# Kernel tuning notes

Measured on AMD Instinct MI355X. Metric: run time of the kernel, lower is better.

Reference implementation:

```python
import jax, jax.numpy as jnp
import numpy as np
from jax import lax

# Dimensions
B, CIN, COUT = 8, 3, 3
NF = 128          # num_features
K = 9             # DISCO kernel_shape (number of filter basis functions)
HLAT, WLON = 181, 360   # in_shape == out_shape (1-degree equiangular sphere grid)
KH, KW = 5, 5     # compact lat/lon support of each DISCO basis function


def setup_inputs() -> dict:
    key = jax.random.key(0)
    ks = jax.random.split(key, 10)
    s = lambda fan: 1.0 / np.sqrt(fan)
    return {
        "x": jax.random.normal(ks[0], (B, CIN, HLAT, WLON), jnp.float32),
        # DISCO conv: latitude-dependent basis filters, quadrature weights, channel mix
        "psi": jax.random.normal(ks[1], (K, HLAT, KH, KW), jnp.float32) * s(KH * KW),
        "quad": jnp.abs(jax.random.normal(ks[2], (HLAT,), jnp.float32)) * (1.0 / HLAT)
                + jnp.sin(jnp.pi * (jnp.arange(HLAT) + 0.5) / HLAT) * (1.0 / HLAT),
        "w1": jax.random.normal(ks[3], (NF, CIN, K), jnp.float32) * s(CIN * K),
        "b1": jnp.zeros((NF,), jnp.float32),
        # standard conv2d stages
        "w2": jax.random.normal(ks[4], (NF // 2, NF, 5, 5), jnp.float32) * s(NF * 25),
        "b2": jnp.zeros((NF // 2,), jnp.float32),
        "w3": jax.random.normal(ks[5], (COUT, NF // 2, 5, 5), jnp.float32) * s(NF // 2 * 25),
        "b3": jnp.zeros((COUT,), jnp.float32),
    }


def _disco_conv_s2(x, psi, quad, w, b):
    """Discrete-continuous spherical conv: latitude-dependent gather + weighted sum.
    x: [B,C,H,W]; psi: [K,H,KH,KW]; quad: [H]; w: [O,C,K]; b: [O] -> [B,O,H,W]"""
    H, W = x.shape[-2], x.shape[-1]
    rh, rw = KH // 2, KW // 2
    xw = x * quad[None, None, :, None]                       # quadrature-weighted input
    # neighborhood indices: clipped in latitude, circular in longitude
    hi = jnp.clip(jnp.arange(H)[:, None] + jnp.arange(KH)[None, :] - rh, 0, H - 1)  # [H,KH]
    wi = (jnp.arange(W)[:, None] + jnp.arange(KW)[None, :] - rw) % W                # [W,KW]
    g = xw[:, :, hi, :]                                      # [B,C,H,KH,W]
    patches = g[:, :, :, :, wi]                              # [B,C,H,KH,W,KW]
    # project onto latitude-dependent filter basis, then mix channels per basis
    z = jnp.einsum('khij,bchiwj->bckhw', psi, patches)       # [B,C,K,H,W]
    return jnp.einsum('ock,bckhw->bohw', w, z) + b[None, :, None, None]


def _conv2d(x, w, b, pad):
    y = lax.conv_general_dilated(x, w, (1, 1), [(pad, pad), (pad, pad)],
                                 dimension_numbers=('NCHW', 'OIHW', 'NCHW'))
    return y + b[None, :, None, None]


def reference(x, psi, quad, w1, b1, w2, b2, w3, b3):
    h = jax.nn.relu(_disco_conv_s2(x, psi, quad, w1, b1))
    h = jax.nn.relu(_conv2d(h, w2, b2, 2))
    return _conv2d(h, w3, b3, 2)
```

## Files before the change

### kernel.cpp

```cpp
#include <hip/hip_runtime.h>
#include <hip/hip_bf16.h>

#define HLAT 181
#define WLON 360
#define HW (HLAT * WLON)
#define HPAD 188
#define WPAD 368
#define PCH ((size_t)HPAD * WPAD * 16)
#define W2P 372
#define PLANE2 ((size_t)HPAD * W2P * 64)
#define ZROW ((size_t)384 * 64)

typedef __attribute__((ext_vector_type(4)))  short short4v;
typedef __attribute__((ext_vector_type(8)))  short short8v;
typedef __attribute__((ext_vector_type(4)))  float f32x4;
typedef __attribute__((ext_vector_type(16))) float f32x16;

static __device__ __forceinline__ ushort bf16_hi_bits(float f) {
  union { float f; unsigned u; } c; c.f = f;
  unsigned u = c.u;
  unsigned rounded = u + 0x7FFF + ((u >> 16) & 1);
  return (ushort)(rounded >> 16);
}
static __device__ __forceinline__ float bf16_to_f(ushort b) {
  union { unsigned u; float f; } c; c.u = ((unsigned)b) << 16;
  return c.f;
}

__global__ __launch_bounds__(256) void k_tw(const float* __restrict__ w2,
                                            const float* __restrict__ w3,
                                            const float* __restrict__ w1,
                                            const float* __restrict__ b1,
                                            ushort* __restrict__ w2f,
                                            ushort* __restrict__ w1f,
                                            ushort* __restrict__ w3f) {
  int idx = blockIdx.x * 256 + threadIdx.x;
  if (idx < 51200) {
    int l   = idx & 63;
    int p   = (idx >> 6) & 1;
    int m   = (idx >> 7) & 1;
    int ch  = (idx >> 8) & 7;
    int tap = idx >> 11;
    int oc  = m * 32 + (l & 31);
    int ci0 = ch * 16 + (l >> 5) * 8;
#pragma unroll
    for (int j = 0; j < 8; ++j) {
      float f = w2[(oc * 128 + ci0 + j) * 25 + tap];
      ushort hi = bf16_hi_bits(f);
      w2f[(size_t)idx * 8 + j] = (p == 0) ? hi : bf16_hi_bits(f - bf16_to_f(hi));
    }
  }
  if (idx < 1024) {
    int l = idx & 63;
    int e = idx >> 6;
    int p  = e & 1;
    int kc = (e >> 1) & 1;
    int m  = e >> 2;
    int oc = m * 32 + (l & 31);
    int k0 = kc * 16 + (l >> 5) * 8;
#pragma unroll
    for (int j = 0; j < 8; ++j) {
      int k = k0 + j;
      float f = (k < 27) ? w1[oc * 27 + k] : (k == 27 ? b1[oc] : 0.f);
      ushort hi = bf16_hi_bits(f);
      w1f[(size_t)idx * 8 + j] = (p == 0) ? hi : bf16_hi_bits(f - bf16_to_f(hi));
    }
  }
  if (idx < 6400) {
    int l   = idx & 63;
    int p   = (idx >> 6) & 1;
    int kc  = (idx >> 7) & 1;
    int tap = idx >> 8;
    int oc  = l & 15;
    int ci0 = kc * 32 + (l >> 4) * 8;
#pragma unroll
    for (int j = 0; j < 8; ++j) {
      float f = (oc < 3) ? w3[(oc * 64 + ci0 + j) * 25 + tap] : 0.f;
      ushort hi = bf16_hi_bits(f);
      w3f[(size_t)idx * 8 + j] = (p == 0) ? hi : bf16_hi_bits(f - bf16_to_f(hi));
    }
  }
}

__global__ __launch_bounds__(256) void k_zring(ushort* __restrict__ h1s) {
  const int i = blockIdx.x * 256 + threadIdx.x;
  if (i >= 4024) return;
  int row, col;
  if (i < 736)       { row = i / 368;              col = i % 368; }
  else if (i < 2576) { int p = i - 736;  row = 183 + p / 368; col = p % 368; }
  else if (i < 2938) { int p = i - 2576; row = 2 + p % 181;   col = p / 181; }
  else               { int p = i - 2938; row = 2 + p % 181;   col = 362 + p / 181; }
  short8v z = {0, 0, 0, 0, 0, 0, 0, 0};
  short8v* d = (short8v*)(h1s + (size_t)blockIdx.y * PCH + ((size_t)row * 368 + col) * 16);
  d[0] = z; d[1] = z;
}

__global__ __launch_bounds__(256) void k_zring2(ushort* __restrict__ h2p) {
  const int i = blockIdx.x * 256 + threadIdx.x;
  if (i >= 4776) return;
  int row, col;
  if (i < 744)       { row = i / W2P;             col = i % W2P; }
  else if (i < 2604) { int p = i - 744;  row = 183 + p / W2P; col = p % W2P; }
  else               { int p = i - 2604; row = 2 + p % 181;
                       int cI = p / 181; col = (cI < 2) ? cI : 360 + cI; }
  short8v z = {0, 0, 0, 0, 0, 0, 0, 0};
  short8v* d = (short8v*)(h2p + (size_t)blockIdx.y * PLANE2 + ((size_t)row * W2P + col) * 64);
#pragma unroll
  for (int k = 0; k < 8; ++k) d[k] = z;
}

__global__ __launch_bounds__(384, 2) void k_z(const float* __restrict__ x,
    const float* __restrict__ psi, const float* __restrict__ quad,
    ushort* __restrict__ zbuf, int b0) {
  const int h = blockIdx.x;
  const int bi = blockIdx.y;
  const int b = b0 + bi;
  const int tid = threadIdx.x;
  ushort* dst = zbuf + (size_t)(bi * HLAT + h) * ZROW + (size_t)tid * 64;
  if (tid >= 360) {
    short8v zz = {0, 0, 0, 0, 0, 0, 0, 0};
    short8v* d8 = (short8v*)dst;
#pragma unroll
    for (int k = 0; k < 8; ++k) d8[k] = zz;
    return;
  }
  float z[28];
#pragma unroll
  for (int q = 0; q < 28; ++q) z[q] = 0.f;
#pragma unroll 1
  for (int i = 0; i < 5; ++i) {
    int hi = h + i - 2;
    hi = hi < 0 ? 0 : (hi >= HLAT ? HLAT - 1 : hi);
    const float qv = quad[hi];
    float pv[45];
#pragma unroll
    for (int kk = 0; kk < 9; ++kk)
#pragma unroll
      for (int j = 0; j < 5; ++j)
        pv[kk * 5 + j] = psi[((size_t)(kk * HLAT + h)) * 25 + i * 5 + j];
#pragma unroll
    for (int c = 0; c < 3; ++c) {
      const float* row = x + ((size_t)(b * 3 + c) * HLAT + hi) * WLON;
      float v[5];
#pragma unroll
      for (int j = 0; j < 5; ++j) {
        int wj = tid + j - 2;
        wj = wj < 0 ? wj + WLON : (wj >= WLON ? wj - WLON : wj);
        v[j] = row[wj] * qv;
      }
#pragma unroll
      for (int kk = 0; kk < 9; ++kk) {
        float a = 0.f;
#pragma unroll
        for (int j = 0; j < 5; ++j) a += pv[kk * 5 + j] * v[j];
        z[c * 9 + kk] += a;
      }
    }
  }
  z[27] = 1.0f;
  ushort hiv[32], lov[32];
#pragma unroll
  for (int q = 0; q < 28; ++q) {
    const ushort hb = bf16_hi_bits(z[q]);
    hiv[q] = hb;
    lov[q] = bf16_hi_bits(z[q] - bf16_to_f(hb));
  }
#pragma unroll
  for (int q = 28; q < 32; ++q) { hiv[q] = 0; lov[q] = 0; }
#pragma unroll
  for (int part = 0; part < 2; ++part)
#pragma unroll
    for (int kc = 0; kc < 2; ++kc)
#pragma unroll
      for (int half = 0; half < 2; ++half) {
        union { ushort u[8]; short8v v8; } t8;
#pragma unroll
        for (int j = 0; j < 8; ++j)
          t8.u[j] = (part == 0 ? hiv : lov)[kc * 16 + half * 8 + j];
        *(short8v*)&dst[part * 32 + kc * 16 + half * 8] = t8.v8;
      }
}

__global__ __launch_bounds__(256, 2) void k_mv(const ushort* __restrict__ zbuf,
    const ushort* __restrict__ w1f, ushort* __restrict__ h1s) {
  const int h = blockIdx.x;
  const int bi = blockIdx.y;
  const int tid = threadIdx.x;
  const int wv = tid >> 6;
  const int l = tid & 63;
  const int l31 = l & 31;
  const int q = l >> 5;
  const short8v* wf1 = (const short8v*)w1f;
  short8v A[4][2][2];
#pragma unroll
  for (int m = 0; m < 4; ++m)
#pragma unroll
    for (int kc = 0; kc < 2; ++kc)
#pragma unroll
      for (int p = 0; p < 2; ++p)
        A[m][kc][p] = wf1[(size_t)(((m * 2 + kc) * 2 + p) * 64 + l)];

  ushort* base = h1s + (size_t)bi * 16 * PCH;
  const ushort* zrow = zbuf + (size_t)(bi * HLAT + h) * ZROW;
#pragma unroll
  for (int nn = 0; nn < 3; ++nn) {
    const int n = wv * 3 + nn;
    const int px = n * 32 + l31;
    const ushort* zp = zrow + (size_t)px * 64 + q * 8;
    const short8v bh0 = *(const short8v*)(zp + 0);
    const short8v bh1 = *(const short8v*)(zp + 16);
    const short8v bl0 = *(const short8v*)(zp + 32);
    const short8v bl1 = *(const short8v*)(zp + 48);
    const bool ok = px < 360;
    const size_t pixoff = ((size_t)(h + 2) * WPAD + (px + 2)) * 16;
#pragma unroll
    for (int m = 0; m < 4; ++m) {
      f32x16 acc;
#pragma unroll
      for (int e = 0; e < 16; ++e) acc[e] = 0.f;
      acc = __builtin_amdgcn_mfma_f32_32x32x16_bf16(A[m][0][0], bh0, acc, 0, 0, 0);
      acc = __builtin_amdgcn_mfma_f32_32x32x16_bf16(A[m][0][1], bh0, acc, 0, 0, 0);
      acc = __builtin_amdgcn_mfma_f32_32x32x16_bf16(A[m][0][0], bl0, acc, 0, 0, 0);
      acc = __builtin_amdgcn_mfma_f32_32x32x16_bf16(A[m][1][0], bh1, acc, 0, 0, 0);
      acc = __builtin_amdgcn_mfma_f32_32x32x16_bf16(A[m][1][1], bh1, acc, 0, 0, 0);
      acc = __builtin_amdgcn_mfma_f32_32x32x16_bf16(A[m][1][0], bl1, acc, 0, 0, 0);
      if (ok) {
#pragma unroll
        for (int r = 0; r < 4; ++r) {
          const int rb = 8 * r + 4 * q;
          const int ch = m * 2 + (rb >> 4);
          const int ci0 = rb & 15;
          short4v h4, l4;
#pragma unroll
          for (int j = 0; j < 4; ++j) {
            const float v = fmaxf(acc[r * 4 + j], 0.f);
            const ushort hb = bf16_hi_bits(v);
            h4[j] = (short)hb;
            l4[j] = (short)bf16_hi_bits(v - bf16_to_f(hb));
          }
          *(short4v*)(base + (size_t)ch * PCH + pixoff + ci0) = h4;
          *(short4v*)(base + (size_t)(8 + ch) * PCH + pixoff + ci0) = l4;
        }
      }
    }
  }
}

__global__ __launch_bounds__(256, 2) void k_conv2(const ushort* __restrict__ h1s,
    const ushort* __restrict__ w2f, const float* __restrict__ b2,
    ushort* __restrict__ h2p) {
  __shared__ ushort act[2][2][12][40][16];
  const int x0 = blockIdx.x * 32;
  const int y0 = blockIdx.y * 8;
  const int bi = blockIdx.z;
  const int tid = threadIdx.x;
  const int wv = tid >> 6;
  const int m  = wv >> 1;
  const int wr = wv & 1;
  const int l = tid & 63;
  const int l31 = l & 31;
  const int q8 = (l >> 5) * 8;

  f32x16 acc[4];
#pragma unroll
  for (int r = 0; r < 4; ++r)
#pragma unroll
    for (int e = 0; e < 16; ++e) acc[r][e] = 0.f;

  const short8v* wf = (const short8v*)w2f;
  const ushort* pbase = h1s + (size_t)bi * 16 * PCH;

  auto stage = [&](int buf, int ch) {
#pragma unroll
    for (int s = 0; s < 12; ++s) {
      const int k = wv * 12 + s;
      const int part = k / 24;
      const int rem = k - part * 24;
      const int t = rem >> 1;
      const int slot = rem & 1;
      const ushort* pl = pbase + (size_t)(part * 8 + ch) * PCH;
      if (slot == 0) {
        const ushort* g = pl + ((size_t)(y0 + t) * WPAD + (x0 + (l >> 1))) * 16 + (l & 1) * 8;
        __builtin_amdgcn_global_load_lds(
            (const __attribute__((address_space(1))) unsigned int*)g,
            (__attribute__((address_space(3))) unsigned int*)&act[buf][part][t][0][0], 16, 0, 0);
      } else {
        const ushort* g = pl + ((size_t)(y0 + t) * WPAD + (x0 + 32 + (l >> 3))) * 16 + (l & 7) * 2;
        __builtin_amdgcn_global_load_lds(
            (const __attribute__((address_space(1))) unsigned int*)g,
            (__attribute__((address_space(3))) unsigned int*)&act[buf][part][t][32][0], 4, 0, 0);
      }
    }
  };

  stage(0, 0);
  asm volatile("s_waitcnt vmcnt(0)" ::: "memory");
  __syncthreads();

#pragma unroll 1
  for (int ch = 0; ch < 8; ++ch) {
    const int cur = ch & 1;
    if (ch < 7) stage(cur ^ 1, ch + 1);
#pragma unroll 1
    for (int dj = 0; dj < 5; ++dj) {
      short8v aw[5][2];
#pragma unroll
      for (int di = 0; di < 5; ++di) {
        const size_t e0 = (size_t)(((di * 5 + dj) * 8 + ch) * 4 + m * 2) * 64 + l;
        aw[di][0] = wf[e0];
        aw[di][1] = wf[e0 + 64];
      }
      __builtin_amdgcn_s_setprio(1);
#pragma unroll
      for (int rr = 0; rr < 8; ++rr) {
        const int t = wr * 4 + rr;
        const int c = l31 + dj;
        const short8v bh = *(const short8v*)&act[cur][0][t][c][q8];
        const short8v bl = *(const short8v*)&act[cur][1][t][c][q8];
#pragma unroll
        for (int di = 0; di < 5; ++di) {
          const int r = rr - di;
          if (r < 0 || r > 3) continue;
          acc[r] = __builtin_amdgcn_mfma_f32_32x32x16_bf16(aw[di][0], bh, acc[r], 0, 0, 0);
          acc[r] = __builtin_amdgcn_mfma_f32_32x32x16_bf16(aw[di][1], bh, acc[r], 0, 0, 0);
          acc[r] = __builtin_amdgcn_mfma_f32_32x32x16_bf16(aw[di][0], bl, acc[r], 0, 0, 0);
        }
      }
      __builtin_amdgcn_s_setprio(0);
    }
    asm volatile("s_waitcnt vmcnt(0)" ::: "memory");
    __syncthreads();
  }

  const int xg = x0 + l31;
  ushort* hp = h2p + (size_t)bi * 2 * PLANE2;
  if (xg < WLON) {
#pragma unroll
    for (int r = 0; r < 4; ++r) {
      const int y = y0 + wr * 4 + r;
      if (y >= HLAT) continue;
      const size_t po = ((size_t)(y + 2) * W2P + (xg + 2)) * 64;
#pragma unroll
      for (int run = 0; run < 4; ++run) {
        const int oc0 = m * 32 + 8 * run + (q8 >> 1);
        short4v h4, l4;
#pragma unroll
        for (int j = 0; j < 4; ++j) {
          const float v = fmaxf(acc[r][run * 4 + j] + b2[oc0 + j], 0.f);
          const ushort hb = bf16_hi_bits(v);
          h4[j] = (short)hb;
          l4[j] = (short)bf16_hi_bits(v - bf16_to_f(hb));
        }
        *(short4v*)(hp + po + oc0) = h4;
        *(short4v*)(hp + PLANE2 + po + oc0) = l4;
      }
    }
  }
}

__global__ __launch_bounds__(256, 2) void k_conv3(const ushort* __restrict__ h2p,
    const ushort* __restrict__ w3f, const float* __restrict__ b3,
    float* __restrict__ out, int b0) {
  __shared__ ushort act[2][12][20][72];
  const int x0 = blockIdx.x * 16;
  const int y0 = blockIdx.y * 8;
  const int bi = blockIdx.z;
  const int tid = threadIdx.x;
  const int wv = tid >> 6;
  const int l = tid & 63;

  {
    const ushort* pb = h2p + (size_t)bi * 2 * PLANE2;
    float4 v[6][3];
#pragma unroll
    for (int pr = 0; pr < 6; ++pr) {
      const int pair = wv * 6 + pr;
      const int part = pair / 12;
      const int row = pair % 12;
      const ushort* src = pb + (size_t)part * PLANE2 +
                          ((size_t)(y0 + row) * W2P + x0) * 64;
      v[pr][0] = *(const float4*)((const char*)src + l * 16);
      v[pr][1] = *(const float4*)((const char*)src + 1024 + l * 16);
      if (l < 32) v[pr][2] = *(const float4*)((const char*)src + 2048 + l * 16);
    }
#pragma unroll
    for (int pr = 0; pr < 6; ++pr) {
      const int pair = wv * 6 + pr;
      const int part = pair / 12;
      const int row = pair % 12;
#pragma unroll
      for (int k2 = 0; k2 < 3; ++k2) {
        if (k2 == 2 && l >= 32) continue;
        const int B = k2 * 1024 + l * 16;
        const int col = B >> 7;
        const int ci = (B & 127) >> 1;
        *(short8v*)&act[part][row][col][ci] = *(short8v*)&v[pr][k2];
      }
    }
  }
  __syncthreads();

  f32x4 acc[2];
#pragma unroll
  for (int r = 0; r < 2; ++r)
#pragma unroll
    for (int e = 0; e < 4; ++e) acc[r][e] = 0.f;

  const short8v* wf3 = (const short8v*)w3f;
  const int c16 = l & 15;
  const int koff0 = ((l >> 4) & 3) * 8;

#pragma unroll 1
  for (int kc = 0; kc < 2; ++kc) {
#pragma unroll 1
    for (int dj = 0; dj < 5; ++dj) {
      short8v A[5][2];
#pragma unroll
      for (int di = 0; di < 5; ++di) {
        const size_t e0 = (size_t)(((di * 5 + dj) * 2 + kc) * 2) * 64 + l;
        A[di][0] = wf3[e0];
        A[di][1] = wf3[e0 + 64];
      }
      const int c = c16 + dj;
      const int koff = kc * 32 + koff0;
      __builtin_amdgcn_s_setprio(1);
#pragma unroll
      for (int tt = 0; tt < 6; ++tt) {
        const int t = wv * 2 + tt;
        const short8v bh = *(const short8v*)&act[0][t][c][koff];
        const short8v bl = *(const short8v*)&act[1][t][c][koff];
#pragma unroll
        for (int di = 0; di < 5; ++di) {
          const int r = tt - di;
          if (r < 0 || r > 1) continue;
          acc[r] = __builtin_amdgcn_mfma_f32_16x16x32_bf16(A[di][0], bh, acc[r], 0, 0, 0);
          acc[r] = __builtin_amdgcn_mfma_f32_16x16x32_bf16(A[di][1], bh, acc[r], 0, 0, 0);
          acc[r] = __builtin_amdgcn_mfma_f32_16x16x32_bf16(A[di][0], bl, acc[r], 0, 0, 0);
        }
      }
      __builtin_amdgcn_s_setprio(0);
    }
  }

  const int px = x0 + c16;
  const int b = b0 + bi;
  if ((l >> 4) == 0 && px < WLON) {
    const float bb[3] = {b3[0], b3[1], b3[2]};
#pragma unroll
    for (int r = 0; r < 2; ++r) {
      const int y = y0 + wv * 2 + r;
      if (y >= HLAT) continue;
#pragma unroll
      for (int j = 0; j < 3; ++j)
        out[((size_t)(b * 3 + j) * HLAT + y) * WLON + px] = acc[r][j] + bb[j];
    }
  }
}

extern "C" void kernel_launch(void* const* d_in, const int* in_sizes, int n_in,
                              void* d_out, int out_size, void* d_ws, size_t ws_size,
                              hipStream_t stream) {
  const float* x    = (const float*)d_in[0];
  const float* psi  = (const float*)d_in[1];
  const float* quad = (const float*)d_in[2];
  const float* w1   = (const float*)d_in[3];
  const float* b1   = (const float*)d_in[4];
  const float* w2   = (const float*)d_in[5];
  const float* b2   = (const float*)d_in[6];
  const float* w3   = (const float*)d_in[7];
  const float* b3   = (const float*)d_in[8];
  float* out = (float*)d_out;
  float* ws  = (float*)d_ws;

  ushort* w2f = (ushort*)ws;
  ushort* w1f = (ushort*)(ws + 204800);
  ushort* w3f = (ushort*)(ws + 208896);
  const size_t HEAD = 234496;

  size_t wsf = ws_size / 4;
  const size_t h1s_f = PCH * 8;
  const size_t h2p_f = PLANE2;
  const size_t per_b = h1s_f + h2p_f;
  int bc = 8;
  while (bc > 1 && HEAD + (size_t)bc * per_b > wsf) bc >>= 1;

  ushort* h1s = (ushort*)(ws + HEAD);
  ushort* h2p = (ushort*)(ws + HEAD + (size_t)bc * h1s_f);
  ushort* zbuf = h2p;

  k_tw<<<dim3(200), dim3(256), 0, stream>>>(w2, w3, w1, b1, w2f, w1f, w3f);
  k_zring<<<dim3(16, bc * 16), dim3(256), 0, stream>>>(h1s);

  for (int b0 = 0; b0 < 8; b0 += bc) {
    int cur = 8 - b0 < bc ? 8 - b0 : bc;
    k_z<<<dim3(HLAT, cur), dim3(384), 0, stream>>>(x, psi, quad, zbuf, b0);
    k_mv<<<dim3(HLAT, cur), dim3(256), 0, stream>>>(zbuf, w1f, h1s);
    k_zring2<<<dim3(19, cur * 2), dim3(256), 0, stream>>>(h2p);
    k_conv2<<<dim3(12, 23, cur), dim3(256), 0, stream>>>(h1s, w2f, b2, h2p);
    k_conv3<<<dim3(23, 23, cur), dim3(256), 0, stream>>>(h2p, w3f, b3, out, b0);
  }
}
```

Before: 768.0 us.

## Tile zbuf layout for coalesced MFMA loads and stage k_mv stores via LDS

Changes the intermediate zbuf from pixel-major 64-element rows into tiled blocks of 32 pixels by 16 elements, so k_mv's B-operand loads are contiguous per wave and k_z writes are tiled accordingly. In k_mv, MFMA results are written to a shared-memory staging buffer and then stored to global as 16-byte vectors per pixel, replacing scattered 8-byte stores. This adds LDS traffic and a per-wave shared buffer, and relies on wave-level ordering without an explicit barrier between the LDS write and read.

```diff
diff --git a/kernel.cpp b/kernel.cpp
--- a/kernel.cpp
+++ b/kernel.cpp
@@ -9,7 +9,7 @@
 #define PCH ((size_t)HPAD * WPAD * 16)
 #define W2P 372
 #define PLANE2 ((size_t)HPAD * W2P * 64)
-#define ZROW ((size_t)384 * 64)
+#define ZROW ((size_t)12 * 4 * 32 * 16)
 
 typedef __attribute__((ext_vector_type(4)))  short short4v;
 typedef __attribute__((ext_vector_type(8)))  short short8v;
@@ -116,48 +116,42 @@
   const int bi = blockIdx.y;
   const int b = b0 + bi;
   const int tid = threadIdx.x;
-  ushort* dst = zbuf + (size_t)(bi * HLAT + h) * ZROW + (size_t)tid * 64;
-  if (tid >= 360) {
-    short8v zz = {0, 0, 0, 0, 0, 0, 0, 0};
-    short8v* d8 = (short8v*)dst;
-#pragma unroll
-    for (int k = 0; k < 8; ++k) d8[k] = zz;
-    return;
-  }
   float z[28];
 #pragma unroll
   for (int q = 0; q < 28; ++q) z[q] = 0.f;
+  if (tid < 360) {
 #pragma unroll 1
-  for (int i = 0; i < 5; ++i) {
-    int hi = h + i - 2;
-    hi = hi < 0 ? 0 : (hi >= HLAT ? HLAT - 1 : hi);
-    const float qv = quad[hi];
-    float pv[45];
-#pragma unroll
-    for (int kk = 0; kk < 9; ++kk)
-#pragma unroll
-      for (int j = 0; j < 5; ++j)
-        pv[kk * 5 + j] = psi[((size_t)(kk * HLAT + h)) * 25 + i * 5 + j];
-#pragma unroll
-    for (int c = 0; c < 3; ++c) {
-      const float* row = x + ((size_t)(b * 3 + c) * HLAT + hi) * WLON;
-      float v[5];
-#pragma unroll
-      for (int j = 0; j < 5; ++j) {
-        int wj = tid + j - 2;
-        wj = wj < 0 ? wj + WLON : (wj >= WLON ? wj - WLON : wj);
-        v[j] = row[wj] * qv;
-      }
-#pragma unroll
-      for (int kk = 0; kk < 9; ++kk) {
-        float a = 0.f;
-#pragma unroll
-        for (int j = 0; j < 5; ++j) a += pv[kk * 5 + j] * v[j];
-        z[c * 9 + kk] += a;
-      }
-    }
-  }
-  z[27] = 1.0f;
+    for (int i = 0; i < 5; ++i) {
+      int hi = h + i - 2;
+      hi = hi < 0 ? 0 : (hi >= HLAT ? HLAT - 1 : hi);
+      const float qv = quad[hi];
+      float pv[45];
+#pragma unroll
+      for (int kk = 0; kk < 9; ++kk)
+#pragma unroll
+        for (int j = 0; j < 5; ++j)
+          pv[kk * 5 + j] = psi[((size_t)(kk * HLAT + h)) * 25 + i * 5 + j];
+#pragma unroll
+      for (int c = 0; c < 3; ++c) {
+        const float* row = x + ((size_t)(b * 3 + c) * HLAT + hi) * WLON;
+        float v[5];
+#pragma unroll
+        for (int j = 0; j < 5; ++j) {
+          int wj = tid + j - 2;
+          wj = wj < 0 ? wj + WLON : (wj >= WLON ? wj - WLON : wj);
+          v[j] = row[wj] * qv;
+        }
+#pragma unroll
+        for (int kk = 0; kk < 9; ++kk) {
+          float a = 0.f;
+#pragma unroll
+          for (int j = 0; j < 5; ++j) a += pv[kk * 5 + j] * v[j];
+          z[c * 9 + kk] += a;
+        }
+      }
+    }
+    z[27] = 1.0f;
+  }
   ushort hiv[32], lov[32];
 #pragma unroll
   for (int q = 0; q < 28; ++q) {
@@ -167,22 +161,23 @@
   }
 #pragma unroll
   for (int q = 28; q < 32; ++q) { hiv[q] = 0; lov[q] = 0; }
-#pragma unroll
-  for (int part = 0; part < 2; ++part)
-#pragma unroll
-    for (int kc = 0; kc < 2; ++kc)
-#pragma unroll
-      for (int half = 0; half < 2; ++half) {
-        union { ushort u[8]; short8v v8; } t8;
-#pragma unroll
-        for (int j = 0; j < 8; ++j)
-          t8.u[j] = (part == 0 ? hiv : lov)[kc * 16 + half * 8 + j];
-        *(short8v*)&dst[part * 32 + kc * 16 + half * 8] = t8.v8;
-      }
+
+  ushort* tb = zbuf + (size_t)(bi * HLAT + h) * ZROW +
+               (size_t)(tid >> 5) * 2048 + (size_t)(tid & 31) * 16;
+#pragma unroll
+  for (int pk = 0; pk < 4; ++pk) {
+    const ushort* src = (pk < 2 ? hiv : lov) + (pk & 1) * 16;
+    union { ushort u[8]; short8v v8; } a0, a1;
+#pragma unroll
+    for (int j = 0; j < 8; ++j) { a0.u[j] = src[j]; a1.u[j] = src[8 + j]; }
+    *(short8v*)(tb + (size_t)pk * 512 + 0) = a0.v8;
+    *(short8v*)(tb + (size_t)pk * 512 + 8) = a1.v8;
+  }
 }
 
 __global__ __launch_bounds__(256, 2) void k_mv(const ushort* __restrict__ zbuf,
     const ushort* __restrict__ w1f, ushort* __restrict__ h1s) {
+  __shared__ ushort st[4][16][32][16];
   const int h = blockIdx.x;
   const int bi = blockIdx.y;
   const int tid = threadIdx.x;
@@ -205,14 +200,11 @@
 #pragma unroll
   for (int nn = 0; nn < 3; ++nn) {
     const int n = wv * 3 + nn;
-    const int px = n * 32 + l31;
-    const ushort* zp = zrow + (size_t)px * 64 + q * 8;
-    const short8v bh0 = *(const short8v*)(zp + 0);
-    const short8v bh1 = *(const short8v*)(zp + 16);
-    const short8v bl0 = *(const short8v*)(zp + 32);
-    const short8v bl1 = *(const short8v*)(zp + 48);
-    const bool ok = px < 360;
-    const size_t pixoff = ((size_t)(h + 2) * WPAD + (px + 2)) * 16;
+    const ushort* zn = zrow + (size_t)n * 2048 + l31 * 16 + q * 8;
+    const short8v bh0 = *(const short8v*)(zn + 0);
+    const short8v bh1 = *(const short8v*)(zn + 512);
+    const short8v bl0 = *(const short8v*)(zn + 1024);
+    const short8v bl1 = *(const short8v*)(zn + 1536);
 #pragma unroll
     for (int m = 0; m < 4; ++m) {
       f32x16 acc;
@@ -224,23 +216,30 @@
       acc = __builtin_amdgcn_mfma_f32_32x32x16_bf16(A[m][1][0], bh1, acc, 0, 0, 0);
       acc = __builtin_amdgcn_mfma_f32_32x32x16_bf16(A[m][1][1], bh1, acc, 0, 0, 0);
       acc = __builtin_amdgcn_mfma_f32_32x32x16_bf16(A[m][1][0], bl1, acc, 0, 0, 0);
-      if (ok) {
-#pragma unroll
-        for (int r = 0; r < 4; ++r) {
-          const int rb = 8 * r + 4 * q;
-          const int ch = m * 2 + (rb >> 4);
-          const int ci0 = rb & 15;
-          short4v h4, l4;
-#pragma unroll
-          for (int j = 0; j < 4; ++j) {
-            const float v = fmaxf(acc[r * 4 + j], 0.f);
-            const ushort hb = bf16_hi_bits(v);
-            h4[j] = (short)hb;
-            l4[j] = (short)bf16_hi_bits(v - bf16_to_f(hb));
-          }
-          *(short4v*)(base + (size_t)ch * PCH + pixoff + ci0) = h4;
-          *(short4v*)(base + (size_t)(8 + ch) * PCH + pixoff + ci0) = l4;
+#pragma unroll
+      for (int r = 0; r < 4; ++r) {
+        const int rb = 8 * r + 4 * q;
+        const int p2h = m * 2 + (rb >> 4);
+        const int ci0 = rb & 15;
+        short4v h4, l4;
+#pragma unroll
+        for (int j = 0; j < 4; ++j) {
+          const float v = fmaxf(acc[r * 4 + j], 0.f);
+          const ushort hb = bf16_hi_bits(v);
+          h4[j] = (short)hb;
+          l4[j] = (short)bf16_hi_bits(v - bf16_to_f(hb));
         }
+        *(short4v*)&st[wv][p2h][l31][ci0] = h4;
+        *(short4v*)&st[wv][8 + p2h][l31][ci0] = l4;
+      }
+    }
+    const int pxr = n * 32 + (l >> 1);
+    if (pxr < 360) {
+      const size_t po = ((size_t)(h + 2) * WPAD + (pxr + 2)) * 16 + (l & 1) * 8;
+#pragma unroll
+      for (int p2 = 0; p2 < 16; ++p2) {
+        const short8v v = *(const short8v*)&st[wv][p2][l >> 1][(l & 1) * 8];
+        *(short8v*)(base + (size_t)p2 * PCH + po) = v;
       }
     }
   }
```

New measurement: 756.9 us. Within noise of the previous version (-1.4%).
